# Optimization experiments

Hardware: AMD Instinct MI355X
Metric: run time of the kernel (lower is better)

The kernel has to match this reference:

```python
import jax, jax.numpy as jnp
import numpy as np

B, S, D = 2, 2048, 2048   # batch, seq, query_dim (= inner_dim)
H, DH = 32, 64            # heads, dim_head
EPS = 1e-6


def _rms_norm(x, g):
    # RMSNorm across the full inner dim ('rms_norm_across_heads')
    var = jnp.mean(x * x, axis=-1, keepdims=True)
    return x * jax.lax.rsqrt(var + EPS) * g


def _rope_interleaved(x, cos, sin):
    # x: [B,S,D]; pairs (even, odd) along last dim
    xp = x.reshape(*x.shape[:-1], -1, 2)
    x_real, x_imag = xp[..., 0], xp[..., 1]
    x_rot = jnp.stack([-x_imag, x_real], axis=-1).reshape(x.shape)
    return x * cos + x_rot * sin


def setup_inputs() -> dict:
    key = jax.random.key(0)
    ks = jax.random.split(key, 12)
    sc = 0.02
    inp = {
        "hidden_states": jax.random.normal(ks[0], (B, S, D), jnp.float32),
        "cos": jax.random.normal(ks[1], (B, S, D), jnp.float32),
        "sin": jax.random.normal(ks[2], (B, S, D), jnp.float32),
        "Wq": jax.random.normal(ks[3], (D, D), jnp.float32) * sc,
        "bq": jnp.zeros((D,), jnp.float32),
        "Wk": jax.random.normal(ks[4], (D, D), jnp.float32) * sc,
        "bk": jnp.zeros((D,), jnp.float32),
        "Wv": jax.random.normal(ks[5], (D, D), jnp.float32) * sc,
        "bv": jnp.zeros((D,), jnp.float32),
        "Wo": jax.random.normal(ks[6], (D, D), jnp.float32) * sc,
        "bo": jnp.zeros((D,), jnp.float32),
        "gq": jnp.ones((D,), jnp.float32),
        "gk": jnp.ones((D,), jnp.float32),
    }
    return inp


def reference(hidden_states, cos, sin, Wq, bq, Wk, bk, Wv, bv, Wo, bo, gq, gk):
    x = hidden_states
    q = _rms_norm(x @ Wq.T + bq, gq)
    k = _rms_norm(x @ Wk.T + bk, gk)
    v = x @ Wv.T + bv
    q = _rope_interleaved(q, cos, sin)
    k = _rope_interleaved(k, cos, sin)
    # split heads: [B,S,H,DH]
    q = q.reshape(B, S, H, DH)
    k = k.reshape(B, S, H, DH)
    v = v.reshape(B, S, H, DH)
    scale = 1.0 / np.sqrt(DH).astype(np.float32)
    scores = jnp.einsum('bqhd,bkhd->bhqk', q, k) * scale
    probs = jax.nn.softmax(scores, axis=-1)
    out = jnp.einsum('bhqk,bkhd->bqhd', probs, v).reshape(B, S, H * DH)
    return out @ Wo.T + bo
```

## Files before the change

kernel.cpp:

```cpp
#include <hip/hip_runtime.h>
#include <cmath>
#include <stdint.h>

typedef unsigned short ushort_t;
typedef __attribute__((ext_vector_type(8))) short bf16x8;
typedef __attribute__((ext_vector_type(4))) float f32x4;
typedef __attribute__((ext_vector_type(16))) float f32x16;

#define LOG2E 1.4426950408889634f

__device__ __forceinline__ float bf2f(unsigned short u) {
    return __uint_as_float(((unsigned)u) << 16);
}
__device__ __forceinline__ unsigned short f2bf(float f) {
    unsigned u = __float_as_uint(f);
    u = u + 0x7fffu + ((u >> 16) & 1u);
    return (unsigned short)(u >> 16);
}
__device__ __forceinline__ unsigned cvt_pk_bf16(float lo, float hi) {
    unsigned r;
    asm("v_cvt_pk_bf16_f32 %0, %1, %2" : "=v"(r) : "v"(lo), "v"(hi));
    return r;
}
__device__ __forceinline__ void gld_lds16(void* lds, const void* g) {
    __builtin_amdgcn_global_load_lds(
        (const __attribute__((address_space(1))) unsigned int*)g,
        (__attribute__((address_space(3))) unsigned int*)lds,
        16, 0, 0);
}

__global__ __launch_bounds__(256) void cast_all(
    const float* __restrict__ x, const float* __restrict__ wq,
    const float* __restrict__ wk, const float* __restrict__ wv,
    const float* __restrict__ wo, const float* __restrict__ bq,
    const float* __restrict__ bk, const float* __restrict__ bv,
    ushort_t* __restrict__ xb, ushort_t* __restrict__ wqkvb,
    ushort_t* __restrict__ wob, float* __restrict__ biasqkv)
{
    const int X4 = 2097152;
    const int W4 = 1048576;
    int i = blockIdx.x * 256 + threadIdx.x;
    if (i < X4) {
        float4 v = ((const float4*)x)[i];
        ushort_t* d = xb + (size_t)i * 4;
        d[0]=f2bf(v.x); d[1]=f2bf(v.y); d[2]=f2bf(v.z); d[3]=f2bf(v.w);
    } else if (i < X4 + 3*W4) {
        int j = i - X4;
        const float* w; int jj;
        if (j < W4)        { w = wq; jj = j; }
        else if (j < 2*W4) { w = wk; jj = j - W4; }
        else               { w = wv; jj = j - 2*W4; }
        float4 v = ((const float4*)w)[jj];
        ushort_t* d = wqkvb + (size_t)j * 4;
        d[0]=f2bf(v.x); d[1]=f2bf(v.y); d[2]=f2bf(v.z); d[3]=f2bf(v.w);
    } else if (i < X4 + 4*W4) {
        int j = i - X4 - 3*W4;
        float4 v = ((const float4*)wo)[j];
        ushort_t* d = wob + (size_t)j * 4;
        d[0]=f2bf(v.x); d[1]=f2bf(v.y); d[2]=f2bf(v.z); d[3]=f2bf(v.w);
    } else {
        int j = i - X4 - 4*W4;
        const float4* s;
        if (j < 512)       s = (const float4*)bq + j;
        else if (j < 1024) s = (const float4*)bk + (j - 512);
        else               s = (const float4*)bv + (j - 1024);
        ((float4*)biasqkv)[j] = *s;
    }
}

template<int OUTF32>
__global__ __launch_bounds__(256, 2) void gemm_bt(
    const ushort_t* __restrict__ A, const ushort_t* __restrict__ Bw,
    const float* __restrict__ bias, void* __restrict__ Cout,
    int M, int N, int K)
{
    __shared__ __align__(16) ushort_t As[128 * 64];
    __shared__ __align__(16) ushort_t Bs[128 * 64];
    const int bn = blockIdx.x, bm = blockIdx.y;
    const int tid = threadIdx.x, w = tid >> 6, l = tid & 63;
    const int wr = w >> 1, wc = w & 1;
    const int g = l >> 4, r = l & 15;
    f32x4 acc[4][4] = {};
    const ushort_t* Ab = A + (size_t)bm * 128 * K + (size_t)(l >> 3) * K + (l & 7) * 8;
    const ushort_t* Bb = Bw + (size_t)bn * 128 * K + (size_t)(l >> 3) * K + (l & 7) * 8;

    for (int kt = 0; kt < K; kt += 64) {
#pragma unroll
        for (int i = 0; i < 4; ++i) {
            const int chunk = i * 4 + w;
            gld_lds16(&As[chunk * 512], Ab + (size_t)(chunk * 8) * K + kt);
            gld_lds16(&Bs[chunk * 512], Bb + (size_t)(chunk * 8) * K + kt);
        }
        asm volatile("s_waitcnt vmcnt(0)" ::: "memory");
        __syncthreads();
#pragma unroll
        for (int kk = 0; kk < 2; ++kk) {
            bf16x8 a[4], b[4];
#pragma unroll
            for (int mi = 0; mi < 4; ++mi)
                a[mi] = *(const bf16x8*)&As[(wr*64 + mi*16 + r) * 64 + kk*32 + g*8];
#pragma unroll
            for (int ni = 0; ni < 4; ++ni)
                b[ni] = *(const bf16x8*)&Bs[(wc*64 + ni*16 + r) * 64 + kk*32 + g*8];
#pragma unroll
            for (int mi = 0; mi < 4; ++mi)
#pragma unroll
                for (int ni = 0; ni < 4; ++ni)
                    acc[mi][ni] = __builtin_amdgcn_mfma_f32_16x16x32_bf16(
                        a[mi], b[ni], acc[mi][ni], 0, 0, 0);
        }
        __syncthreads();
    }
#pragma unroll
    for (int mi = 0; mi < 4; ++mi) {
#pragma unroll
        for (int ni = 0; ni < 4; ++ni) {
            const int col = bn*128 + wc*64 + ni*16 + r;
            const float bc = bias[col];
#pragma unroll
            for (int j = 0; j < 4; ++j) {
                const int row = bm*128 + wr*64 + mi*16 + 4*g + j;
                const float v = acc[mi][ni][j] + bc;
                if (OUTF32) ((float*)Cout)[(size_t)row * N + col] = v;
                else        ((ushort_t*)Cout)[(size_t)row * N + col] = f2bf(v);
            }
        }
    }
}

__global__ __launch_bounds__(256) void prep_qk(
    const ushort_t* __restrict__ qkvb, const float* __restrict__ cosb,
    const float* __restrict__ sinb, const float* __restrict__ gq,
    const float* __restrict__ gk, ushort_t* __restrict__ qfr,
    ushort_t* __restrict__ kfr)
{
    const int row = blockIdx.x;
    const int b = row >> 11, s = row & 2047;
    const int t = threadIdx.x, w = t >> 6, l = t & 63;
    const int d0 = t * 8;
    const ushort_t* qr = qkvb + (size_t)row * 6144 + d0;
    bf16x8 qv = *(const bf16x8*)qr;
    bf16x8 kv = *(const bf16x8*)(qr + 2048);
    float qf[8], kf[8];
#pragma unroll
    for (int j = 0; j < 8; ++j) {
        qf[j] = bf2f((unsigned short)qv[j]);
        kf[j] = bf2f((unsigned short)kv[j]);
    }
    float sq = 0.f, sk = 0.f;
#pragma unroll
    for (int j = 0; j < 8; ++j) { sq += qf[j]*qf[j]; sk += kf[j]*kf[j]; }
#pragma unroll
    for (int off = 1; off < 64; off <<= 1) {
        sq += __shfl_xor(sq, off);
        sk += __shfl_xor(sk, off);
    }
    __shared__ float red[2][4];
    if (l == 0) { red[0][w] = sq; red[1][w] = sk; }
    __syncthreads();
    sq = red[0][0] + red[0][1] + red[0][2] + red[0][3];
    sk = red[1][0] + red[1][1] + red[1][2] + red[1][3];
    const float rq = rsqrtf(sq * (1.f/2048.f) + 1e-6f);
    const float rk = rsqrtf(sk * (1.f/2048.f) + 1e-6f);

    const float* cp = cosb + (size_t)row * 2048 + d0;
    const float* sp = sinb + (size_t)row * 2048 + d0;
    float4 c0 = *(const float4*)cp,       c1 = *(const float4*)(cp + 4);
    float4 s0 = *(const float4*)sp,       s1 = *(const float4*)(sp + 4);
    float4 g0 = *(const float4*)(gq + d0), g1 = *(const float4*)(gq + d0 + 4);
    float4 h0 = *(const float4*)(gk + d0), h1 = *(const float4*)(gk + d0 + 4);
    float cf[8] = {c0.x,c0.y,c0.z,c0.w,c1.x,c1.y,c1.z,c1.w};
    float sf[8] = {s0.x,s0.y,s0.z,s0.w,s1.x,s1.y,s1.z,s1.w};
    float gqa[8] = {g0.x,g0.y,g0.z,g0.w,g1.x,g1.y,g1.z,g1.w};
    float gka[8] = {h0.x,h0.y,h0.z,h0.w,h1.x,h1.y,h1.z,h1.w};

    const float QSC = 0.125f * LOG2E;
    bf16x8 qo, ko;
#pragma unroll
    for (int p = 0; p < 4; ++p) {
        const int e = 2*p, o = 2*p + 1;
        const float qe = qf[e]*rq*gqa[e], qod = qf[o]*rq*gqa[o];
        const float ke = kf[e]*rk*gka[e], kod = kf[o]*rk*gka[o];
        qo[e] = (short)f2bf((qe*cf[e] - qod*sf[e]) * QSC);
        qo[o] = (short)f2bf((qod*cf[o] + qe*sf[o]) * QSC);
        ko[e] = (short)f2bf(ke*cf[e] - kod*sf[e]);
        ko[o] = (short)f2bf(kod*cf[o] + ke*sf[o]);
    }
    const int h = d0 >> 6;
    const int dh0 = d0 & 63;
    const int tf = (dh0 >> 4) & 3, b5 = (dh0 >> 3) & 1;
    const int lane = b5 * 32 + (s & 31);
    const int tile = s >> 5;
    const size_t oidx = ((((size_t)b*32 + h) * 64 + tile) * 4 + tf) * 512 + lane * 8;
    *(bf16x8*)(qfr + oidx) = qo;
    *(bf16x8*)(kfr + oidx) = ko;
}

__global__ __launch_bounds__(256) void vfrag(
    const ushort_t* __restrict__ qkvb, ushort_t* __restrict__ vf)
{
    const int blk = blockIdx.x;
    const int bh = blk >> 5, kvt = blk & 31;
    const int b = bh >> 5, h = bh & 31;
    __shared__ ushort_t tile[64][72];
    const int tid = threadIdx.x;
#pragma unroll
    for (int it = 0; it < 2; ++it) {
        const int chunk = it * 256 + tid;
        const int sl = chunk >> 3, dp = (chunk & 7) * 8;
        bf16x8 v = *(const bf16x8*)&qkvb[(size_t)(b*2048 + kvt*64 + sl) * 6144 + 4096 + h*64 + dp];
        *(bf16x8*)&tile[sl][dp] = v;
    }
    __syncthreads();
#pragma unroll
    for (int it = 0; it < 2; ++it) {
        const int oc = it * 256 + tid;
        const int dt = oc >> 8, s = (oc >> 6) & 3, lane = oc & 63;
        const int b5 = lane >> 5, r5 = lane & 31;
        bf16x8 o;
#pragma unroll
        for (int j = 0; j < 8; ++j)
            o[j] = (short)tile[16*s + 8*b5 + j][32*dt + r5];
        *(bf16x8*)&vf[((((size_t)bh*32 + kvt)*2 + dt)*4 + s)*512 + lane*8] = o;
    }
}

__global__ __launch_bounds__(128, 3) void attn_fwd(
    const ushort_t* __restrict__ qfr, const ushort_t* __restrict__ kfr,
    const ushort_t* __restrict__ vf, ushort_t* __restrict__ aout)
{
    const int bid = blockIdx.x;
    const int xcd = bid & 7, li = bid >> 3;
    const int bh = xcd * 8 + (li >> 5);
    const int qblk = li & 31;
    const int tid = threadIdx.x, w = tid >> 6, l = tid & 63;
    const int b5 = l >> 5, r5 = l & 31;
    const int qt = qblk * 2 + w;

    const ushort_t* qbase = qfr + (((size_t)bh * 64 + qt) * 4) * 512 + l * 8;
    const ushort_t* kbase = kfr + ((size_t)bh * 64 * 4) * 512 + l * 8;
    const ushort_t* vbase = vf + ((size_t)bh * 32 * 8) * 512 + l * 8;

    bf16x8 q[4];
#pragma unroll
    for (int t = 0; t < 4; ++t)
        q[t] = *(const bf16x8*)(qbase + t * 512);

    f32x16 ot[2];
#pragma unroll
    for (int dt = 0; dt < 2; ++dt)
#pragma unroll
        for (int i = 0; i < 16; ++i) ot[dt][i] = 0.f;
    float lsum = 0.f;

    auto loadk = [&](bf16x8 (&ka)[4], int idxh) {
#pragma unroll
        for (int t = 0; t < 4; ++t)
            ka[t] = *(const bf16x8*)(kbase + ((size_t)idxh * 4 + t) * 512);
    };

    auto body = [&](const bf16x8 (&ka)[4], int idxh) {
        bf16x8 va[2][2];
#pragma unroll
        for (int sl = 0; sl < 2; ++sl)
#pragma unroll
            for (int dt = 0; dt < 2; ++dt)
                va[sl][dt] = *(const bf16x8*)(vbase +
                    (((size_t)(idxh >> 1) * 2 + dt) * 4 + 2 * (idxh & 1) + sl) * 512);

        f32x16 st;
#pragma unroll
        for (int i = 0; i < 16; ++i) st[i] = -16.f;
#pragma unroll
        for (int t = 0; t < 4; ++t)
            st = __builtin_amdgcn_mfma_f32_32x32x16_bf16(ka[t], q[t], st, 0, 0, 0);

        unsigned pk[8];
        float ls0 = 0.f, ls1 = 0.f;
#pragma unroll
        for (int p = 0; p < 8; ++p) {
            const float lo = exp2f(st[2*p]);
            const float hi = exp2f(st[2*p+1]);
            if (p & 1) ls1 += lo + hi; else ls0 += lo + hi;
            pk[p] = cvt_pk_bf16(lo, hi);
        }
        lsum += ls0 + ls1;

#pragma unroll
        for (int sl = 0; sl < 2; ++sl) {
            const unsigned X0 = pk[4*sl+0], X1 = pk[4*sl+1];
            const unsigned Y0 = pk[4*sl+2], Y1 = pk[4*sl+3];
            const unsigned sX0 = (unsigned)__shfl_xor((int)X0, 32);
            const unsigned sX1 = (unsigned)__shfl_xor((int)X1, 32);
            const unsigned sY0 = (unsigned)__shfl_xor((int)Y0, 32);
            const unsigned sY1 = (unsigned)__shfl_xor((int)Y1, 32);
            union { unsigned u[4]; bf16x8 v; } pb;
            pb.u[0] = b5 ? sY0 : X0;
            pb.u[1] = b5 ? sY1 : X1;
            pb.u[2] = b5 ? Y0 : sX0;
            pb.u[3] = b5 ? Y1 : sX1;
            ot[0] = __builtin_amdgcn_mfma_f32_32x32x16_bf16(va[sl][0], pb.v, ot[0], 0, 0, 0);
            ot[1] = __builtin_amdgcn_mfma_f32_32x32x16_bf16(va[sl][1], pb.v, ot[1], 0, 0, 0);
        }
    };

    bf16x8 kaA[4], kaB[4];
    loadk(kaA, 0);
    for (int kt = 0; kt < 32; ++kt) {
        loadk(kaB, 2*kt + 1);
        body(kaA, 2*kt);
        const int nx = (kt == 31) ? 0 : (2*kt + 2);
        loadk(kaA, nx);
        body(kaB, 2*kt + 1);
    }

    const float prs = __shfl_xor(lsum, 32);
    const float rinv = 1.f / (lsum + prs);
    const int b = bh >> 5, h = bh & 31;
    const int sq = qt * 32 + r5;
    ushort_t* orow = aout + ((size_t)b * 2048 + sq) * 2048 + h * 64;
#pragma unroll
    for (int dt = 0; dt < 2; ++dt)
#pragma unroll
        for (int rb = 0; rb < 4; ++rb) {
            ushort4 pk4;
            pk4.x = f2bf(ot[dt][4*rb+0] * rinv);
            pk4.y = f2bf(ot[dt][4*rb+1] * rinv);
            pk4.z = f2bf(ot[dt][4*rb+2] * rinv);
            pk4.w = f2bf(ot[dt][4*rb+3] * rinv);
            *(ushort4*)(orow + 32*dt + 8*rb + 4*b5) = pk4;
        }
}

extern "C" void kernel_launch(void* const* d_in, const int* in_sizes, int n_in,
                              void* d_out, int out_size, void* d_ws, size_t ws_size,
                              hipStream_t stream) {
    const float* x    = (const float*)d_in[0];
    const float* cosb = (const float*)d_in[1];
    const float* sinb = (const float*)d_in[2];
    const float* Wq   = (const float*)d_in[3];
    const float* bq   = (const float*)d_in[4];
    const float* Wk   = (const float*)d_in[5];
    const float* bk   = (const float*)d_in[6];
    const float* Wv   = (const float*)d_in[7];
    const float* bv   = (const float*)d_in[8];
    const float* Wo   = (const float*)d_in[9];
    const float* bo   = (const float*)d_in[10];
    const float* gq   = (const float*)d_in[11];
    const float* gk   = (const float*)d_in[12];

    char* W = (char*)d_ws;
    ushort_t* xb      = (ushort_t*)(W);
    ushort_t* wqkvb   = (ushort_t*)(W + 16777216);
    ushort_t* wob     = (ushort_t*)(W + 41943040);
    float*    biasqkv = (float*)   (W + 50331648);
    ushort_t* qkvb    = (ushort_t*)(W + 50356224);
    ushort_t* qfb     = (ushort_t*)(W + 100687872);
    ushort_t* kfb     = (ushort_t*)(W + 117465088);
    ushort_t* vfb     = (ushort_t*)(W + 134242304);
    ushort_t* attnb   = xb;

    cast_all<<<24582, 256, 0, stream>>>(x, Wq, Wk, Wv, Wo, bq, bk, bv,
                                        xb, wqkvb, wob, biasqkv);
    gemm_bt<0><<<dim3(48, 32), 256, 0, stream>>>(xb, wqkvb, biasqkv, qkvb,
                                                 4096, 6144, 2048);
    prep_qk<<<4096, 256, 0, stream>>>(qkvb, cosb, sinb, gq, gk, qfb, kfb);
    vfrag<<<2048, 256, 0, stream>>>(qkvb, vfb);
    attn_fwd<<<2048, 128, 0, stream>>>(qfb, kfb, vfb, attnb);
    gemm_bt<1><<<dim3(16, 32), 256, 0, stream>>>(attnb, wob, bo, (float*)d_out,
                                                 4096, 2048, 2048);
}
```

Baseline: 507.2 us.

## Use 256x256-tile double-buffered GEMM with XCD swizzle for QKV projection

Adds a new bf16 MFMA GEMM kernel that uses 256x256 output tiles, 512 threads, double-buffered LDS with direct global-to-LDS loads and an XOR-swizzled LDS layout. Blocks are remapped so consecutive tiles land on the same XCD. The kernel replaces the 128x128 GEMM for the fused QKV projection. The larger tile means more data reuse per LDS load, but it needs 128 KB of LDS and many accumulator registers, which lowers occupancy. The grid of 384 blocks may also leave some compute units underused.

```diff
diff --git a/kernel.cpp b/kernel.cpp
--- a/kernel.cpp
+++ b/kernel.cpp
@@ -128,6 +128,109 @@
     }
 }
 
+template<int OUTF32>
+__global__ __launch_bounds__(512, 2) void gemm256(
+    const ushort_t* __restrict__ A, const ushort_t* __restrict__ Bw,
+    const float* __restrict__ bias, void* __restrict__ Cout,
+    int M, int N, int K)
+{
+    __shared__ __align__(16) ushort_t lds[2][512 * 64];
+    const int nbx = N >> 8;
+    const int nwg = gridDim.x;
+    const int bid = blockIdx.x;
+    const int cpx = nwg >> 3;
+    const int swz = (bid & 7) * cpx + (bid >> 3);
+    const int bn = swz % nbx, bm = swz / nbx;
+
+    const int tid = threadIdx.x, w = tid >> 6, l = tid & 63;
+    const int wm = w >> 2, wn = w & 3;
+    const int g = l >> 4, r = l & 15;
+    const int NT = K >> 6;
+
+    const int lrow8 = l >> 3;
+    const int cbyte = ((l & 7) ^ lrow8) << 4;
+    const ushort_t* Abase = A  + (size_t)(bm*256 + w*8 + lrow8) * K + (cbyte >> 1);
+    const ushort_t* Bbase = Bw + (size_t)(bn*256 + w*8 + lrow8) * K + (cbyte >> 1);
+
+    auto stage = [&](int buf, int kt) {
+        const ushort_t* ak = Abase + kt * 64;
+        const ushort_t* bk = Bbase + kt * 64;
+        char* lb = (char*)&lds[buf][0] + w * 1024;
+#pragma unroll
+        for (int i = 0; i < 4; ++i)
+            gld_lds16(lb + i * 8192, ak + (size_t)(i * 64) * K);
+#pragma unroll
+        for (int i = 0; i < 4; ++i)
+            gld_lds16(lb + 32768 + i * 8192, bk + (size_t)(i * 64) * K);
+    };
+
+    f32x4 acc[8][4] = {};
+    const int rowA = wm * 128;
+    const int rowB = 256 + wn * 64;
+    const int cb0 = (g * 16) ^ ((r & 7) << 4);
+    const int cb1 = (64 + g * 16) ^ ((r & 7) << 4);
+
+    stage(0, 0);
+    for (int kt = 0; kt < NT; ++kt) {
+        const int p = kt & 1;
+        if (kt + 1 < NT) {
+            stage(p ^ 1, kt + 1);
+            asm volatile("s_waitcnt vmcnt(8)" ::: "memory");
+        } else {
+            asm volatile("s_waitcnt vmcnt(0)" ::: "memory");
+        }
+        asm volatile("s_barrier" ::: "memory");
+
+        const char* lb = (const char*)&lds[p][0];
+        bf16x8 a0[8], b0[4], a1[8], b1[4];
+#pragma unroll
+        for (int mi = 0; mi < 8; ++mi)
+            a0[mi] = *(const bf16x8*)(lb + (rowA + mi*16 + r) * 128 + cb0);
+#pragma unroll
+        for (int ni = 0; ni < 4; ++ni)
+            b0[ni] = *(const bf16x8*)(lb + (rowB + ni*16 + r) * 128 + cb0);
+#pragma unroll
+        for (int mi = 0; mi < 8; ++mi)
+            a1[mi] = *(const bf16x8*)(lb + (rowA + mi*16 + r) * 128 + cb1);
+#pragma unroll
+        for (int ni = 0; ni < 4; ++ni)
+            b1[ni] = *(const bf16x8*)(lb + (rowB + ni*16 + r) * 128 + cb1);
+
+#pragma unroll
+        for (int mi = 0; mi < 8; ++mi)
+#pragma unroll
+            for (int ni = 0; ni < 4; ++ni)
+                acc[mi][ni] = __builtin_amdgcn_mfma_f32_16x16x32_bf16(
+                    a0[mi], b0[ni], acc[mi][ni], 0, 0, 0);
+#pragma unroll
+        for (int mi = 0; mi < 8; ++mi)
+#pragma unroll
+            for (int ni = 0; ni < 4; ++ni)
+                acc[mi][ni] = __builtin_amdgcn_mfma_f32_16x16x32_bf16(
+                    a1[mi], b1[ni], acc[mi][ni], 0, 0, 0);
+
+        asm volatile("s_waitcnt lgkmcnt(0)" ::: "memory");
+        __builtin_amdgcn_sched_barrier(0);
+        asm volatile("s_barrier" ::: "memory");
+    }
+
+#pragma unroll
+    for (int mi = 0; mi < 8; ++mi) {
+#pragma unroll
+        for (int ni = 0; ni < 4; ++ni) {
+            const int col = bn*256 + wn*64 + ni*16 + r;
+            const float bc = bias[col];
+#pragma unroll
+            for (int j = 0; j < 4; ++j) {
+                const int row = bm*256 + wm*128 + mi*16 + 4*g + j;
+                const float v = acc[mi][ni][j] + bc;
+                if (OUTF32) ((float*)Cout)[(size_t)row * N + col] = v;
+                else        ((ushort_t*)Cout)[(size_t)row * N + col] = f2bf(v);
+            }
+        }
+    }
+}
+
 __global__ __launch_bounds__(256) void prep_qk(
     const ushort_t* __restrict__ qkvb, const float* __restrict__ cosb,
     const float* __restrict__ sinb, const float* __restrict__ gq,
@@ -362,8 +465,8 @@
 
     cast_all<<<24582, 256, 0, stream>>>(x, Wq, Wk, Wv, Wo, bq, bk, bv,
                                         xb, wqkvb, wob, biasqkv);
-    gemm_bt<0><<<dim3(48, 32), 256, 0, stream>>>(xb, wqkvb, biasqkv, qkvb,
-                                                 4096, 6144, 2048);
+    gemm256<0><<<384, 512, 0, stream>>>(xb, wqkvb, biasqkv, qkvb,
+                                        4096, 6144, 2048);
     prep_qk<<<4096, 256, 0, stream>>>(qkvb, cosb, sinb, gq, gk, qfb, kfb);
     vfrag<<<2048, 256, 0, stream>>>(qkvb, vfb);
     attn_fwd<<<2048, 128, 0, stream>>>(qfb, kfb, vfb, attnb);
```

Measured after the change: 520.2 us. +2.6%, slower.
